# Performance work log

Hardware: AMD Instinct MI355X
Metric: run time of the kernel (lower is better)

Reference implementation:

```python
import jax, jax.numpy as jnp
import numpy as np

B, C, N = 32, 1024, 256   # N=256 is hard-coded by query/key Conv1d in_channels
DQ = 256 // 4             # 64
EPS = 1e-5                # BatchNorm eps


def setup_inputs() -> dict:
    key = jax.random.key(0)
    ks = jax.random.split(key, 16)
    def bn_params(k, ch):
        k1, k2, k3, k4 = jax.random.split(k, 4)
        return (jax.random.uniform(k1, (ch,), jnp.float32, 0.5, 1.5),   # gamma
                jax.random.normal(k2, (ch,), jnp.float32) * 0.1,        # beta
                jax.random.normal(k3, (ch,), jnp.float32) * 0.1,        # running mean
                jax.random.uniform(k4, (ch,), jnp.float32, 0.5, 1.5))   # running var
    bn1 = bn_params(ks[4], DQ)
    bn2 = bn_params(ks[5], DQ)
    bn3 = bn_params(ks[6], C)
    return {
        "x": jax.random.normal(ks[0], (B, C, N), jnp.float32),
        "Wq": jax.random.normal(ks[1], (DQ, N), jnp.float32) * (1.0 / np.sqrt(N)),
        "Wk": jax.random.normal(ks[2], (DQ, N), jnp.float32) * (1.0 / np.sqrt(N)),
        "Wv": jax.random.normal(ks[3], (C, C), jnp.float32) * (1.0 / np.sqrt(C)),
        "bn1_g": bn1[0], "bn1_b": bn1[1], "bn1_m": bn1[2], "bn1_v": bn1[3],
        "bn2_g": bn2[0], "bn2_b": bn2[1], "bn2_m": bn2[2], "bn2_v": bn2[3],
        "bn3_g": bn3[0], "bn3_b": bn3[1], "bn3_m": bn3[2], "bn3_v": bn3[3],
        "alpha": jnp.full((1,), 0.1, jnp.float32),  # torch init is 0; 0.1 keeps the branch active
    }


def _bn(y, g, b, m, v):
    # eval-mode BatchNorm1d over channel axis 1 of (B, ch, L)
    scale = g / jnp.sqrt(v + EPS)
    return (y - m[None, :, None]) * scale[None, :, None] + b[None, :, None]


def reference(x, Wq, Wk, Wv,
              bn1_g, bn1_b, bn1_m, bn1_v,
              bn2_g, bn2_b, bn2_m, bn2_v,
              bn3_g, bn3_b, bn3_m, bn3_v,
              alpha):
    x_hat = jnp.swapaxes(x, 1, 2)                                   # (B, N, C)
    q = jax.nn.relu(_bn(jnp.einsum('on,bnc->boc', Wq, x_hat), bn1_g, bn1_b, bn1_m, bn1_v))  # (B, DQ, C)
    k = jax.nn.relu(_bn(jnp.einsum('on,bnc->boc', Wk, x_hat), bn2_g, bn2_b, bn2_m, bn2_v))  # (B, DQ, C)
    sim = jnp.einsum('bkc,bkd->bcd', k, q)                          # (B, C, C) channel affinity
    aff = jax.nn.softmax(jnp.max(sim, axis=-1, keepdims=True) - sim, axis=-1)
    v = jax.nn.relu(_bn(jnp.einsum('oc,bcn->bon', Wv, x), bn3_g, bn3_b, bn3_m, bn3_v))      # (B, C, N)
    out = jnp.einsum('bcd,bdn->bcn', aff, v)                        # (B, C, N)
    return alpha * out + x
```

## Files before the change

### kernel.cpp

```cpp
#include <hip/hip_runtime.h>
#include <hip/hip_bf16.h>

#define B_  32
#define C_  1024
#define N_  256
#define DQ_ 64

typedef __bf16 bf16_t;
typedef __bf16 bf16x8 __attribute__((ext_vector_type(8)));
typedef float  f32x4  __attribute__((ext_vector_type(4)));

static __device__ __forceinline__ f32x4 mfma16(bf16x8 a, bf16x8 b, f32x4 c) {
  return __builtin_amdgcn_mfma_f32_16x16x32_bf16(a, b, c, 0, 0, 0);
}

static __device__ __forceinline__ bf16x8 ldcvt(const float* p) {
  const float4 a = *(const float4*)p;
  const float4 b = *(const float4*)(p + 4);
  bf16x8 r;
  r[0] = (bf16_t)a.x; r[1] = (bf16_t)a.y; r[2] = (bf16_t)a.z; r[3] = (bf16_t)a.w;
  r[4] = (bf16_t)b.x; r[5] = (bf16_t)b.y; r[6] = (bf16_t)b.z; r[7] = (bf16_t)b.w;
  return r;
}

static __device__ __forceinline__ void stage32(const bf16_t* grow0, size_t gstride,
                                               bf16_t* tile, int wave, int lane) {
#pragma unroll
  for (int t = 0; t < 4; ++t) {
    const int rb = wave * 32 + t * 8;
    const int r  = rb + (lane >> 3);
    const int g  = ((lane & 7) - r) & 7;
    const bf16_t* src = grow0 + (size_t)r * gstride + g * 8;
    __builtin_amdgcn_global_load_lds(
        (const __attribute__((address_space(1))) void*)src,
        (__attribute__((address_space(3))) void*)(tile + rb * 64), 16, 0, 0);
  }
}

__global__ __launch_bounds__(256) void k_trans(const float* __restrict__ x,
                                               bf16_t* __restrict__ xT) {
  __shared__ bf16_t tile[32][34];
  const int b  = blockIdx.z;
  const int n0 = blockIdx.x * 32, c0 = blockIdx.y * 32;
  const int tx = threadIdx.x, ty = threadIdx.y;
  const float* xb = x + (size_t)b * C_ * N_;
  bf16_t*     xtb = xT + (size_t)b * N_ * C_;
#pragma unroll
  for (int i = 0; i < 4; ++i)
    tile[ty + i * 8][tx] = (bf16_t)xb[(size_t)(c0 + ty + i * 8) * N_ + (n0 + tx)];
  __syncthreads();
#pragma unroll
  for (int i = 0; i < 4; ++i)
    xtb[(size_t)(n0 + ty + i * 8) * C_ + (c0 + tx)] = tile[tx][ty + i * 8];
}

__global__ __launch_bounds__(256) void k_cvt(const float* __restrict__ Wv,
                                             const float* __restrict__ Wq,
                                             const float* __restrict__ Wk,
                                             bf16_t* __restrict__ Wvb,
                                             bf16_t* __restrict__ Wqkb) {
  const int gid = blockIdx.x * 256 + threadIdx.x;
  if (blockIdx.x < 512) {
    const int i = gid * 8;
    *(bf16x8*)(Wvb + i) = ldcvt(Wv + i);
  } else {
    const int g2 = (gid - 512 * 256) * 8;
    if (g2 < 16384) *(bf16x8*)(Wqkb + g2) = ldcvt(Wq + g2);
    else            *(bf16x8*)(Wqkb + g2) = ldcvt(Wk + (g2 - 16384));
  }
}

__global__ __launch_bounds__(256) void k_qk(const float* __restrict__ x,
                                            const bf16_t* __restrict__ Wqkb,
                                            const float* __restrict__ g1,
                                            const float* __restrict__ b1,
                                            const float* __restrict__ m1,
                                            const float* __restrict__ v1,
                                            const float* __restrict__ g2,
                                            const float* __restrict__ b2,
                                            const float* __restrict__ m2,
                                            const float* __restrict__ v2,
                                            bf16_t* __restrict__ qt,
                                            bf16_t* __restrict__ kt) {
  const int tid  = threadIdx.x;
  const int wave = tid >> 6;
  const int lane = tid & 63;
  const int quad = lane >> 4;
  const int l16  = lane & 15;
  const int b    = blockIdx.y;
  const int c16  = blockIdx.x * 64 + wave * 16;
  const float* xb = x + (size_t)b * C_ * N_;

  f32x4 acc[8];
#pragma unroll
  for (int i = 0; i < 8; ++i) acc[i] = (f32x4){0.f, 0.f, 0.f, 0.f};

  for (int ks = 0; ks < 8; ++ks) {
    const int k0 = ks * 32 + quad * 8;
    const bf16x8 bx = ldcvt(xb + (size_t)(c16 + l16) * N_ + k0);
#pragma unroll
    for (int i = 0; i < 8; ++i) {
      const bf16x8 aw = *(const bf16x8*)(Wqkb + (size_t)(i * 16 + l16) * N_ + k0);
      acc[i] = mfma16(aw, bx, acc[i]);
    }
  }

#pragma unroll
  for (int i = 0; i < 8; ++i) {
    const bool isq = (i < 4);
    bf16_t* dst = isq ? qt : kt;
#pragma unroll
    for (int r = 0; r < 4; ++r) {
      const int o = (i & 3) * 16 + quad * 4 + r;
      const float sc = (isq ? g1[o] : g2[o]) * rsqrtf((isq ? v1[o] : v2[o]) + 1e-5f);
      const float mm = isq ? m1[o] : m2[o];
      const float bt = isq ? b1[o] : b2[o];
      const int c = c16 + l16;
      float y = (acc[i][r] - mm) * sc + bt;
      y = fmaxf(y, 0.f);
      dst[((size_t)b * C_ + c) * DQ_ + o] = (bf16_t)y;
    }
  }
}

__global__ __launch_bounds__(256, 2) void k_vgemm(const bf16_t* __restrict__ Wvb,
                                                  const bf16_t* __restrict__ xT,
                                                  const float* __restrict__ g,
                                                  const float* __restrict__ be,
                                                  const float* __restrict__ mu,
                                                  const float* __restrict__ va,
                                                  bf16_t* __restrict__ vT) {
  __shared__ __align__(16) bf16_t As[2][128 * 64];
  __shared__ __align__(16) bf16_t Bs[2][128 * 64];
  const int tid  = threadIdx.x;
  const int wave = tid >> 6;
  const int lane = tid & 63;
  const int quad = lane >> 4;
  const int l16  = lane & 15;
  const int o0 = blockIdx.x * 128;
  const int r0 = blockIdx.y * 128;
  const bf16_t* Ab = Wvb + (size_t)o0 * C_;
  const bf16_t* Bb = xT + (size_t)r0 * C_;
  const int wr = (wave >> 1) * 64, wc = (wave & 1) * 64;

  stage32(Ab, C_, (bf16_t*)As[0], wave, lane);
  stage32(Bb, C_, (bf16_t*)Bs[0], wave, lane);

  f32x4 acc[4][4];
#pragma unroll
  for (int i = 0; i < 4; ++i)
#pragma unroll
    for (int j = 0; j < 4; ++j) acc[i][j] = (f32x4){0.f, 0.f, 0.f, 0.f};

  for (int ks = 0; ks < 16; ++ks) {
    __syncthreads();
    const bf16_t* ca = As[ks & 1];
    const bf16_t* cb = Bs[ks & 1];
    if (ks < 15) {
      stage32(Ab + (ks + 1) * 64, C_, (bf16_t*)As[(ks + 1) & 1], wave, lane);
      stage32(Bb + (ks + 1) * 64, C_, (bf16_t*)Bs[(ks + 1) & 1], wave, lane);
    }
#pragma unroll
    for (int ksub = 0; ksub < 2; ++ksub) {
      bf16x8 a[4], bfr[4];
#pragma unroll
      for (int i = 0; i < 4; ++i) {
        const int r = wr + i * 16 + l16;
        const int s = ((ksub * 4 + quad) + r) & 7;
        a[i] = *(const bf16x8*)(ca + r * 64 + s * 8);
      }
#pragma unroll
      for (int j = 0; j < 4; ++j) {
        const int r = wc + j * 16 + l16;
        const int s = ((ksub * 4 + quad) + r) & 7;
        bfr[j] = *(const bf16x8*)(cb + r * 64 + s * 8);
      }
#pragma unroll
      for (int i = 0; i < 4; ++i)
#pragma unroll
        for (int j = 0; j < 4; ++j)
          acc[i][j] = mfma16(a[i], bfr[j], acc[i][j]);
    }
  }

#pragma unroll
  for (int i = 0; i < 4; ++i)
#pragma unroll
    for (int r = 0; r < 4; ++r) {
      const int o = o0 + wr + i * 16 + quad * 4 + r;
      const float sc = g[o] * rsqrtf(va[o] + 1e-5f);
      const float mm = mu[o], bt = be[o];
#pragma unroll
      for (int j = 0; j < 4; ++j) {
        const int rG = r0 + wc + j * 16 + l16;
        float y = (acc[i][j][r] - mm) * sc + bt;
        y = fmaxf(y, 0.f);
        vT[(size_t)rG * C_ + o] = (bf16_t)y;
      }
    }
}

static __device__ __forceinline__ int eaddr(int c, int d) {
  const int ch = d >> 3;
  const int ph = (ch & ~7) | ((ch + c) & 7);
  return (c << 10) + (ph << 3) + (d & 7);
}

__global__ __launch_bounds__(512, 2) void k_fused(const bf16_t* __restrict__ qt,
                                                  const bf16_t* __restrict__ kt,
                                                  const bf16_t* __restrict__ vT,
                                                  const float* __restrict__ x,
                                                  const float* __restrict__ alphap,
                                                  float* __restrict__ out) {
  __shared__ __align__(16) bf16_t ebuf[32 * 1024];
  __shared__ __align__(16) bf16_t vs[2][256 * 64];
  __shared__ float redmin[8][32];
  __shared__ float redsum[8][32];
  __shared__ float rowmin[32];
  __shared__ float rowrinv[32];

  const int tid  = threadIdx.x;
  const int wave = tid >> 6;
  const int lane = tid & 63;
  const int quad = lane >> 4;
  const int l16  = lane & 15;
  const int id   = blockIdx.x;
  const int b    = ((id & 7) << 2) | (id >> 8);
  const int c0   = ((id >> 3) & 31) << 5;

  const bf16_t* qb  = qt + (size_t)b * C_ * DQ_;
  const bf16_t* ktb = kt + ((size_t)b * C_ + c0) * DQ_;

  bf16x8 am[2][2];
#pragma unroll
  for (int i = 0; i < 2; ++i)
#pragma unroll
    for (int ksub = 0; ksub < 2; ++ksub)
      am[i][ksub] = *(const bf16x8*)(ktb + (size_t)(i * 16 + l16) * DQ_ + ksub * 32 + quad * 8);

  stage32(qb, DQ_, (bf16_t*)vs[0], wave, lane);
  f32x4 sim[2][8];
#pragma unroll
  for (int i = 0; i < 2; ++i)
#pragma unroll
    for (int nt = 0; nt < 8; ++nt) sim[i][nt] = (f32x4){0.f, 0.f, 0.f, 0.f};

  for (int t = 0; t < 4; ++t) {
    __syncthreads();
    const bf16_t* cur = vs[t & 1];
    if (t < 3) stage32(qb + (size_t)(t + 1) * 256 * DQ_, DQ_, (bf16_t*)vs[(t + 1) & 1], wave, lane);
#pragma unroll
    for (int jn = 0; jn < 2; ++jn) {
      const int r = wave * 32 + jn * 16 + l16;
#pragma unroll
      for (int ksub = 0; ksub < 2; ++ksub) {
        const int s = ((ksub * 4 + quad) + r) & 7;
        const bf16x8 bq = *(const bf16x8*)(cur + r * 64 + s * 8);
        sim[0][t * 2 + jn] = mfma16(am[0][ksub], bq, sim[0][t * 2 + jn]);
        sim[1][t * 2 + jn] = mfma16(am[1][ksub], bq, sim[1][t * 2 + jn]);
      }
    }
  }

  const bf16_t* vb = vT + (size_t)b * N_ * C_;
  stage32(vb, C_, (bf16_t*)vs[0], wave, lane);

  float pmin[2][4];
#pragma unroll
  for (int i = 0; i < 2; ++i)
#pragma unroll
    for (int r = 0; r < 4; ++r) pmin[i][r] = sim[i][0][r];
#pragma unroll
  for (int nt = 1; nt < 8; ++nt)
#pragma unroll
    for (int i = 0; i < 2; ++i)
#pragma unroll
      for (int r = 0; r < 4; ++r) pmin[i][r] = fminf(pmin[i][r], sim[i][nt][r]);
#pragma unroll
  for (int m = 1; m < 16; m <<= 1)
#pragma unroll
    for (int i = 0; i < 2; ++i)
#pragma unroll
      for (int r = 0; r < 4; ++r) pmin[i][r] = fminf(pmin[i][r], __shfl_xor(pmin[i][r], m));
  if (l16 == 0)
#pragma unroll
    for (int i = 0; i < 2; ++i)
#pragma unroll
      for (int r = 0; r < 4; ++r) redmin[wave][i * 16 + quad * 4 + r] = pmin[i][r];
  __syncthreads();
  if (tid < 32) {
    float v = redmin[0][tid];
#pragma unroll
    for (int w = 1; w < 8; ++w) v = fminf(v, redmin[w][tid]);
    rowmin[tid] = v;
  }
  __syncthreads();

  float mn[2][4], psum[2][4];
#pragma unroll
  for (int i = 0; i < 2; ++i)
#pragma unroll
    for (int r = 0; r < 4; ++r) {
      mn[i][r] = rowmin[i * 16 + quad * 4 + r];
      psum[i][r] = 0.f;
    }
#pragma unroll
  for (int nt = 0; nt < 8; ++nt) {
    const int d = ((nt >> 1) << 8) + wave * 32 + ((nt & 1) << 4) + l16;
#pragma unroll
    for (int i = 0; i < 2; ++i)
#pragma unroll
      for (int r = 0; r < 4; ++r) {
        const int c = i * 16 + quad * 4 + r;
        const float e = __expf(mn[i][r] - sim[i][nt][r]);
        ebuf[eaddr(c, d)] = (bf16_t)e;
        psum[i][r] += e;
      }
  }
#pragma unroll
  for (int m = 1; m < 16; m <<= 1)
#pragma unroll
    for (int i = 0; i < 2; ++i)
#pragma unroll
      for (int r = 0; r < 4; ++r) psum[i][r] += __shfl_xor(psum[i][r], m);
  if (l16 == 0)
#pragma unroll
    for (int i = 0; i < 2; ++i)
#pragma unroll
      for (int r = 0; r < 4; ++r) redsum[wave][i * 16 + quad * 4 + r] = psum[i][r];
  __syncthreads();
  if (tid < 32) {
    float s = redsum[0][tid];
#pragma unroll
    for (int w = 1; w < 8; ++w) s += redsum[w][tid];
    rowrinv[tid] = 1.f / s;
  }

  f32x4 oacc[2][2];
#pragma unroll
  for (int i = 0; i < 2; ++i)
#pragma unroll
    for (int jn = 0; jn < 2; ++jn) oacc[i][jn] = (f32x4){0.f, 0.f, 0.f, 0.f};

  for (int ks = 0; ks < 16; ++ks) {
    __syncthreads();
    const bf16_t* cur = vs[ks & 1];
    if (ks < 15) stage32(vb + (ks + 1) * 64, C_, (bf16_t*)vs[(ks + 1) & 1], wave, lane);
#pragma unroll
    for (int ksub = 0; ksub < 2; ++ksub) {
      const int gch = ks * 8 + ksub * 4 + quad;
      const int ph  = (gch & ~7) | ((gch + l16) & 7);
      const bf16x8 ae0 = *(const bf16x8*)(ebuf + ((size_t)l16 << 10) + ph * 8);
      const bf16x8 ae1 = *(const bf16x8*)(ebuf + ((size_t)(16 + l16) << 10) + ph * 8);
#pragma unroll
      for (int jn = 0; jn < 2; ++jn) {
        const int r = wave * 32 + jn * 16 + l16;
        const int s = ((ksub * 4 + quad) + r) & 7;
        const bf16x8 bv = *(const bf16x8*)(cur + r * 64 + s * 8);
        oacc[0][jn] = mfma16(ae0, bv, oacc[0][jn]);
        oacc[1][jn] = mfma16(ae1, bv, oacc[1][jn]);
      }
    }
  }

  const float alpha = alphap[0];
#pragma unroll
  for (int i = 0; i < 2; ++i)
#pragma unroll
    for (int jn = 0; jn < 2; ++jn)
#pragma unroll
      for (int r = 0; r < 4; ++r) {
        const int c = c0 + i * 16 + quad * 4 + r;
        const int n = wave * 32 + jn * 16 + l16;
        const size_t idx = ((size_t)b * C_ + c) * N_ + n;
        out[idx] = alpha * (oacc[i][jn][r] * rowrinv[i * 16 + quad * 4 + r]) + x[idx];
      }
}

extern "C" void kernel_launch(void* const* d_in, const int* in_sizes, int n_in,
                              void* d_out, int out_size, void* d_ws, size_t ws_size,
                              hipStream_t stream) {
  const float* x    = (const float*)d_in[0];
  const float* Wq   = (const float*)d_in[1];
  const float* Wk   = (const float*)d_in[2];
  const float* Wv   = (const float*)d_in[3];
  const float* bn1g = (const float*)d_in[4];
  const float* bn1b = (const float*)d_in[5];
  const float* bn1m = (const float*)d_in[6];
  const float* bn1v = (const float*)d_in[7];
  const float* bn2g = (const float*)d_in[8];
  const float* bn2b = (const float*)d_in[9];
  const float* bn2m = (const float*)d_in[10];
  const float* bn2v = (const float*)d_in[11];
  const float* bn3g = (const float*)d_in[12];
  const float* bn3b = (const float*)d_in[13];
  const float* bn3m = (const float*)d_in[14];
  const float* bn3v = (const float*)d_in[15];
  const float* alph = (const float*)d_in[16];
  float* outp = (float*)d_out;

  char* ws = (char*)d_ws;
  bf16_t* qt   = (bf16_t*)(ws);
  bf16_t* kt   = (bf16_t*)(ws + (size_t)(4u << 20));
  bf16_t* vT   = (bf16_t*)(ws + (size_t)(8u << 20));
  bf16_t* xT   = (bf16_t*)(ws + (size_t)(24u << 20));
  bf16_t* Wvb  = (bf16_t*)(ws + (size_t)(40u << 20));
  bf16_t* Wqkb = (bf16_t*)(ws + (size_t)(42u << 20));

  k_trans<<<dim3(8, 32, 32), dim3(32, 8, 1), 0, stream>>>(x, xT);
  k_cvt<<<dim3(528), 256, 0, stream>>>(Wv, Wq, Wk, Wvb, Wqkb);
  k_qk<<<dim3(16, 32), 256, 0, stream>>>(x, Wqkb,
                                         bn1g, bn1b, bn1m, bn1v,
                                         bn2g, bn2b, bn2m, bn2v, qt, kt);
  k_vgemm<<<dim3(8, 64), 256, 0, stream>>>(Wvb, xT, bn3g, bn3b, bn3m, bn3v, vT);
  k_fused<<<dim3(1024), 512, 0, stream>>>(qt, kt, vT, x, alph, outp);
}
```

Baseline: 251.0 us.

## Restructure fused attention to 16-row tiles with per-wave V staging; LDS-stage Wqk

The fused softmax-affinity kernel now handles 16 channel rows per block with 256 threads and 2048 blocks. Each wave computes sim against its own 256-column slice of q, loaded directly from global memory. Each wave also double-buffers its own 64-row slice of V through LDS using vmcnt waits, so the block-wide barriers inside the K loop are gone. The k_qk kernel now stages the Wq/Wk weights into swizzled LDS once and preloads x fragments, instead of re-reading weights from global memory on every k-step. In exchange, q is read from global memory twice as often overall, the finer split means more blocks, and k_qk needs 64KB of LDS, which limits its occupancy.

```diff
diff --git a/kernel.cpp b/kernel.cpp
--- a/kernel.cpp
+++ b/kernel.cpp
@@ -23,19 +23,7 @@
   return r;
 }
 
-static __device__ __forceinline__ void stage32(const bf16_t* grow0, size_t gstride,
-                                               bf16_t* tile, int wave, int lane) {
-#pragma unroll
-  for (int t = 0; t < 4; ++t) {
-    const int rb = wave * 32 + t * 8;
-    const int r  = rb + (lane >> 3);
-    const int g  = ((lane & 7) - r) & 7;
-    const bf16_t* src = grow0 + (size_t)r * gstride + g * 8;
-    __builtin_amdgcn_global_load_lds(
-        (const __attribute__((address_space(1))) void*)src,
-        (__attribute__((address_space(3))) void*)(tile + rb * 64), 16, 0, 0);
-  }
-}
+#define WAIT_VMCNT(N) __builtin_amdgcn_s_waitcnt(0x0F70 | (N))
 
 __global__ __launch_bounds__(256) void k_trans(const float* __restrict__ x,
                                                bf16_t* __restrict__ xT) {
@@ -82,6 +70,7 @@
                                             const float* __restrict__ v2,
                                             bf16_t* __restrict__ qt,
                                             bf16_t* __restrict__ kt) {
+  __shared__ __align__(16) bf16_t Ws[128 * 256];
   const int tid  = threadIdx.x;
   const int wave = tid >> 6;
   const int lane = tid & 63;
@@ -91,17 +80,38 @@
   const int c16  = blockIdx.x * 64 + wave * 16;
   const float* xb = x + (size_t)b * C_ * N_;
 
+#pragma unroll
+  for (int t = 0; t < 16; ++t) {
+    const int o = wave * 32 + t * 2 + (lane >> 5);
+    const int s = lane & 31;
+    const int g = (s - o) & 31;
+    const bf16_t* src = Wqkb + (size_t)o * N_ + g * 8;
+    __builtin_amdgcn_global_load_lds(
+        (const __attribute__((address_space(1))) void*)src,
+        (__attribute__((address_space(3))) void*)(Ws + (wave * 32 + t * 2) * N_ + lane * 8),
+        16, 0, 0);
+  }
+
+  bf16x8 bx[8];
+#pragma unroll
+  for (int ks = 0; ks < 8; ++ks)
+    bx[ks] = ldcvt(xb + (size_t)(c16 + l16) * N_ + ks * 32 + quad * 8);
+
+  __syncthreads();
+
   f32x4 acc[8];
 #pragma unroll
   for (int i = 0; i < 8; ++i) acc[i] = (f32x4){0.f, 0.f, 0.f, 0.f};
 
+#pragma unroll
   for (int ks = 0; ks < 8; ++ks) {
-    const int k0 = ks * 32 + quad * 8;
-    const bf16x8 bx = ldcvt(xb + (size_t)(c16 + l16) * N_ + k0);
+    const int ch = ks * 4 + quad;
 #pragma unroll
     for (int i = 0; i < 8; ++i) {
-      const bf16x8 aw = *(const bf16x8*)(Wqkb + (size_t)(i * 16 + l16) * N_ + k0);
-      acc[i] = mfma16(aw, bx, acc[i]);
+      const int orow = i * 16 + l16;
+      const int s = (ch + orow) & 31;
+      const bf16x8 aw = *(const bf16x8*)(Ws + (size_t)orow * N_ + s * 8);
+      acc[i] = mfma16(aw, bx[ks], acc[i]);
     }
   }
 
@@ -120,6 +130,20 @@
       y = fmaxf(y, 0.f);
       dst[((size_t)b * C_ + c) * DQ_ + o] = (bf16_t)y;
     }
+  }
+}
+
+static __device__ __forceinline__ void stage32(const bf16_t* grow0, size_t gstride,
+                                               bf16_t* tile, int wave, int lane) {
+#pragma unroll
+  for (int t = 0; t < 4; ++t) {
+    const int rb = wave * 32 + t * 8;
+    const int r  = rb + (lane >> 3);
+    const int g  = ((lane & 7) - r) & 7;
+    const bf16_t* src = grow0 + (size_t)r * gstride + g * 8;
+    __builtin_amdgcn_global_load_lds(
+        (const __attribute__((address_space(1))) void*)src,
+        (__attribute__((address_space(3))) void*)(tile + rb * 64), 16, 0, 0);
   }
 }
 
@@ -200,24 +224,24 @@
     }
 }
 
-static __device__ __forceinline__ int eaddr(int c, int d) {
+static __device__ __forceinline__ int eaddr16(int c, int d) {
   const int ch = d >> 3;
   const int ph = (ch & ~7) | ((ch + c) & 7);
   return (c << 10) + (ph << 3) + (d & 7);
 }
 
-__global__ __launch_bounds__(512, 2) void k_fused(const bf16_t* __restrict__ qt,
+__global__ __launch_bounds__(256, 2) void k_fused(const bf16_t* __restrict__ qt,
                                                   const bf16_t* __restrict__ kt,
                                                   const bf16_t* __restrict__ vT,
                                                   const float* __restrict__ x,
                                                   const float* __restrict__ alphap,
                                                   float* __restrict__ out) {
-  __shared__ __align__(16) bf16_t ebuf[32 * 1024];
-  __shared__ __align__(16) bf16_t vs[2][256 * 64];
-  __shared__ float redmin[8][32];
-  __shared__ float redsum[8][32];
-  __shared__ float rowmin[32];
-  __shared__ float rowrinv[32];
+  __shared__ __align__(16) bf16_t ebuf[16 * 1024];
+  __shared__ __align__(16) bf16_t vs[2][4][64 * 32];
+  __shared__ float redmin[4][16];
+  __shared__ float redsum[4][16];
+  __shared__ float rowmin[16];
+  __shared__ float rowrinv[16];
 
   const int tid  = threadIdx.x;
   const int wave = tid >> 6;
@@ -225,156 +249,134 @@
   const int quad = lane >> 4;
   const int l16  = lane & 15;
   const int id   = blockIdx.x;
-  const int b    = ((id & 7) << 2) | (id >> 8);
-  const int c0   = ((id >> 3) & 31) << 5;
-
+  const int b    = ((id & 7) << 2) | (id >> 9);
+  const int c0   = ((id >> 3) & 63) << 4;
+  const int dbase = wave * 256;
+
+  const bf16_t* ktb = kt + ((size_t)b * C_ + c0) * DQ_;
   const bf16_t* qb  = qt + (size_t)b * C_ * DQ_;
-  const bf16_t* ktb = kt + ((size_t)b * C_ + c0) * DQ_;
-
-  bf16x8 am[2][2];
-#pragma unroll
-  for (int i = 0; i < 2; ++i)
-#pragma unroll
-    for (int ksub = 0; ksub < 2; ++ksub)
-      am[i][ksub] = *(const bf16x8*)(ktb + (size_t)(i * 16 + l16) * DQ_ + ksub * 32 + quad * 8);
-
-  stage32(qb, DQ_, (bf16_t*)vs[0], wave, lane);
-  f32x4 sim[2][8];
-#pragma unroll
-  for (int i = 0; i < 2; ++i)
-#pragma unroll
-    for (int nt = 0; nt < 8; ++nt) sim[i][nt] = (f32x4){0.f, 0.f, 0.f, 0.f};
-
+  bf16x8 am[2];
+  am[0] = *(const bf16x8*)(ktb + (size_t)l16 * DQ_ + quad * 8);
+  am[1] = *(const bf16x8*)(ktb + (size_t)l16 * DQ_ + 32 + quad * 8);
+  f32x4 sim[16];
+#pragma unroll
+  for (int nt = 0; nt < 16; ++nt) {
+    const bf16_t* qrow = qb + (size_t)(dbase + nt * 16 + l16) * DQ_ + quad * 8;
+    const bf16x8 b0 = *(const bf16x8*)(qrow);
+    const bf16x8 b1 = *(const bf16x8*)(qrow + 32);
+    f32x4 acc = (f32x4){0.f, 0.f, 0.f, 0.f};
+    acc = mfma16(am[0], b0, acc);
+    acc = mfma16(am[1], b1, acc);
+    sim[nt] = acc;
+  }
+
+  const bf16_t* vb = vT + ((size_t)b * N_ + wave * 64) * C_;
+  bf16_t* myvs[2] = {(bf16_t*)vs[0][wave], (bf16_t*)vs[1][wave]};
+#pragma unroll
   for (int t = 0; t < 4; ++t) {
-    __syncthreads();
-    const bf16_t* cur = vs[t & 1];
-    if (t < 3) stage32(qb + (size_t)(t + 1) * 256 * DQ_, DQ_, (bf16_t*)vs[(t + 1) & 1], wave, lane);
-#pragma unroll
-    for (int jn = 0; jn < 2; ++jn) {
-      const int r = wave * 32 + jn * 16 + l16;
-#pragma unroll
-      for (int ksub = 0; ksub < 2; ++ksub) {
-        const int s = ((ksub * 4 + quad) + r) & 7;
-        const bf16x8 bq = *(const bf16x8*)(cur + r * 64 + s * 8);
-        sim[0][t * 2 + jn] = mfma16(am[0][ksub], bq, sim[0][t * 2 + jn]);
-        sim[1][t * 2 + jn] = mfma16(am[1][ksub], bq, sim[1][t * 2 + jn]);
+    const int r = t * 16 + (lane >> 2);
+    const int gg = ((lane & 3) - (r + (r >> 2))) & 3;
+    const bf16_t* src = vb + (size_t)r * C_ + gg * 8;
+    __builtin_amdgcn_global_load_lds(
+        (const __attribute__((address_space(1))) void*)src,
+        (__attribute__((address_space(3))) void*)(myvs[0] + t * 512 + lane * 8),
+        16, 0, 0);
+  }
+
+  float pmin[4];
+#pragma unroll
+  for (int r = 0; r < 4; ++r) pmin[r] = sim[0][r];
+#pragma unroll
+  for (int nt = 1; nt < 16; ++nt)
+#pragma unroll
+    for (int r = 0; r < 4; ++r) pmin[r] = fminf(pmin[r], sim[nt][r]);
+#pragma unroll
+  for (int m = 1; m < 16; m <<= 1)
+#pragma unroll
+    for (int r = 0; r < 4; ++r) pmin[r] = fminf(pmin[r], __shfl_xor(pmin[r], m));
+  if (l16 == 0)
+#pragma unroll
+    for (int r = 0; r < 4; ++r) redmin[wave][quad * 4 + r] = pmin[r];
+  __syncthreads();
+  if (tid < 16)
+    rowmin[tid] = fminf(fminf(redmin[0][tid], redmin[1][tid]),
+                        fminf(redmin[2][tid], redmin[3][tid]));
+  __syncthreads();
+
+  float mn[4], psum[4] = {0.f, 0.f, 0.f, 0.f};
+#pragma unroll
+  for (int r = 0; r < 4; ++r) mn[r] = rowmin[quad * 4 + r];
+#pragma unroll
+  for (int nt = 0; nt < 16; ++nt) {
+    const int d = dbase + nt * 16 + l16;
+#pragma unroll
+    for (int r = 0; r < 4; ++r) {
+      const int c = quad * 4 + r;
+      const float e = __expf(mn[r] - sim[nt][r]);
+      ebuf[eaddr16(c, d)] = (bf16_t)e;
+      psum[r] += e;
+    }
+  }
+#pragma unroll
+  for (int m = 1; m < 16; m <<= 1)
+#pragma unroll
+    for (int r = 0; r < 4; ++r) psum[r] += __shfl_xor(psum[r], m);
+  if (l16 == 0)
+#pragma unroll
+    for (int r = 0; r < 4; ++r) redsum[wave][quad * 4 + r] = psum[r];
+  __syncthreads();
+  if (tid < 16)
+    rowrinv[tid] = 1.f / (redsum[0][tid] + redsum[1][tid] + redsum[2][tid] + redsum[3][tid]);
+  __syncthreads();
+
+  f32x4 oacc[4];
+#pragma unroll
+  for (int jn = 0; jn < 4; ++jn) oacc[jn] = (f32x4){0.f, 0.f, 0.f, 0.f};
+
+  for (int ks = 0; ks < 32; ++ks) {
+    const bf16_t* cur = myvs[ks & 1];
+    if (ks < 31) {
+      bf16_t* nxt = myvs[(ks + 1) & 1];
+      const int koff = (ks + 1) * 32;
+#pragma unroll
+      for (int t = 0; t < 4; ++t) {
+        const int r = t * 16 + (lane >> 2);
+        const int gg = ((lane & 3) - (r + (r >> 2))) & 3;
+        const bf16_t* src = vb + (size_t)r * C_ + koff + gg * 8;
+        __builtin_amdgcn_global_load_lds(
+            (const __attribute__((address_space(1))) void*)src,
+            (__attribute__((address_space(3))) void*)(nxt + t * 512 + lane * 8),
+            16, 0, 0);
       }
-    }
-  }
-
-  const bf16_t* vb = vT + (size_t)b * N_ * C_;
-  stage32(vb, C_, (bf16_t*)vs[0], wave, lane);
-
-  float pmin[2][4];
-#pragma unroll
-  for (int i = 0; i < 2; ++i)
-#pragma unroll
-    for (int r = 0; r < 4; ++r) pmin[i][r] = sim[i][0][r];
-#pragma unroll
-  for (int nt = 1; nt < 8; ++nt)
-#pragma unroll
-    for (int i = 0; i < 2; ++i)
-#pragma unroll
-      for (int r = 0; r < 4; ++r) pmin[i][r] = fminf(pmin[i][r], sim[i][nt][r]);
-#pragma unroll
-  for (int m = 1; m < 16; m <<= 1)
-#pragma unroll
-    for (int i = 0; i < 2; ++i)
-#pragma unroll
-      for (int r = 0; r < 4; ++r) pmin[i][r] = fminf(pmin[i][r], __shfl_xor(pmin[i][r], m));
-  if (l16 == 0)
-#pragma unroll
-    for (int i = 0; i < 2; ++i)
-#pragma unroll
-      for (int r = 0; r < 4; ++r) redmin[wave][i * 16 + quad * 4 + r] = pmin[i][r];
-  __syncthreads();
-  if (tid < 32) {
-    float v = redmin[0][tid];
-#pragma unroll
-    for (int w = 1; w < 8; ++w) v = fminf(v, redmin[w][tid]);
-    rowmin[tid] = v;
-  }
-  __syncthreads();
-
-  float mn[2][4], psum[2][4];
-#pragma unroll
-  for (int i = 0; i < 2; ++i)
+      WAIT_VMCNT(4);
+    } else {
+      WAIT_VMCNT(0);
+    }
+    const int gch = ks * 4 + quad;
+    const int ph  = (gch & ~7) | ((gch + l16) & 7);
+    const bf16x8 ae = *(const bf16x8*)(ebuf + ((size_t)l16 << 10) + ph * 8);
+    bf16x8 bv[4];
+#pragma unroll
+    for (int jn = 0; jn < 4; ++jn) {
+      const int rl = jn * 16 + l16;
+      const int s = (quad + rl + (rl >> 2)) & 3;
+      bv[jn] = *(const bf16x8*)(cur + rl * 32 + s * 8);
+    }
+#pragma unroll
+    for (int jn = 0; jn < 4; ++jn)
+      oacc[jn] = mfma16(ae, bv[jn], oacc[jn]);
+  }
+
+  const float alpha = alphap[0];
+#pragma unroll
+  for (int jn = 0; jn < 4; ++jn)
 #pragma unroll
     for (int r = 0; r < 4; ++r) {
-      mn[i][r] = rowmin[i * 16 + quad * 4 + r];
-      psum[i][r] = 0.f;
-    }
-#pragma unroll
-  for (int nt = 0; nt < 8; ++nt) {
-    const int d = ((nt >> 1) << 8) + wave * 32 + ((nt & 1) << 4) + l16;
-#pragma unroll
-    for (int i = 0; i < 2; ++i)
-#pragma unroll
-      for (int r = 0; r < 4; ++r) {
-        const int c = i * 16 + quad * 4 + r;
-        const float e = __expf(mn[i][r] - sim[i][nt][r]);
-        ebuf[eaddr(c, d)] = (bf16_t)e;
-        psum[i][r] += e;
-      }
-  }
-#pragma unroll
-  for (int m = 1; m < 16; m <<= 1)
-#pragma unroll
-    for (int i = 0; i < 2; ++i)
-#pragma unroll
-      for (int r = 0; r < 4; ++r) psum[i][r] += __shfl_xor(psum[i][r], m);
-  if (l16 == 0)
-#pragma unroll
-    for (int i = 0; i < 2; ++i)
-#pragma unroll
-      for (int r = 0; r < 4; ++r) redsum[wave][i * 16 + quad * 4 + r] = psum[i][r];
-  __syncthreads();
-  if (tid < 32) {
-    float s = redsum[0][tid];
-#pragma unroll
-    for (int w = 1; w < 8; ++w) s += redsum[w][tid];
-    rowrinv[tid] = 1.f / s;
-  }
-
-  f32x4 oacc[2][2];
-#pragma unroll
-  for (int i = 0; i < 2; ++i)
-#pragma unroll
-    for (int jn = 0; jn < 2; ++jn) oacc[i][jn] = (f32x4){0.f, 0.f, 0.f, 0.f};
-
-  for (int ks = 0; ks < 16; ++ks) {
-    __syncthreads();
-    const bf16_t* cur = vs[ks & 1];
-    if (ks < 15) stage32(vb + (ks + 1) * 64, C_, (bf16_t*)vs[(ks + 1) & 1], wave, lane);
-#pragma unroll
-    for (int ksub = 0; ksub < 2; ++ksub) {
-      const int gch = ks * 8 + ksub * 4 + quad;
-      const int ph  = (gch & ~7) | ((gch + l16) & 7);
-      const bf16x8 ae0 = *(const bf16x8*)(ebuf + ((size_t)l16 << 10) + ph * 8);
-      const bf16x8 ae1 = *(const bf16x8*)(ebuf + ((size_t)(16 + l16) << 10) + ph * 8);
-#pragma unroll
-      for (int jn = 0; jn < 2; ++jn) {
-        const int r = wave * 32 + jn * 16 + l16;
-        const int s = ((ksub * 4 + quad) + r) & 7;
-        const bf16x8 bv = *(const bf16x8*)(cur + r * 64 + s * 8);
-        oacc[0][jn] = mfma16(ae0, bv, oacc[0][jn]);
-        oacc[1][jn] = mfma16(ae1, bv, oacc[1][jn]);
-      }
-    }
-  }
-
-  const float alpha = alphap[0];
-#pragma unroll
-  for (int i = 0; i < 2; ++i)
-#pragma unroll
-    for (int jn = 0; jn < 2; ++jn)
-#pragma unroll
-      for (int r = 0; r < 4; ++r) {
-        const int c = c0 + i * 16 + quad * 4 + r;
-        const int n = wave * 32 + jn * 16 + l16;
-        const size_t idx = ((size_t)b * C_ + c) * N_ + n;
-        out[idx] = alpha * (oacc[i][jn][r] * rowrinv[i * 16 + quad * 4 + r]) + x[idx];
-      }
+      const int c = c0 + quad * 4 + r;
+      const int n = wave * 64 + jn * 16 + l16;
+      const size_t idx = ((size_t)b * C_ + c) * N_ + n;
+      out[idx] = alpha * (oacc[jn][r] * rowrinv[quad * 4 + r]) + x[idx];
+    }
 }
 
 extern "C" void kernel_launch(void* const* d_in, const int* in_sizes, int n_in,
@@ -413,5 +415,5 @@
                                          bn1g, bn1b, bn1m, bn1v,
                                          bn2g, bn2b, bn2m, bn2v, qt, kt);
   k_vgemm<<<dim3(8, 64), 256, 0, stream>>>(Wvb, xT, bn3g, bn3b, bn3m, bn3v, vT);
-  k_fused<<<dim3(1024), 512, 0, stream>>>(qt, kt, vT, x, alph, outp);
-}
+  k_fused<<<dim3(2048), 256, 0, stream>>>(qt, kt, vT, x, alph, outp);
+}
```

Result: slower. 256.7 us (+2.3%).
